# Optimization experiments

Hardware: AMD Instinct MI355X
Metric: run time of the kernel (lower is better)

## Reference

```python
import jax, jax.numpy as jnp
import numpy as np

C, W = 144, 9225          # channel_count, batch_width
KW, F = 10, 64            # kernel_width, fc_segment_length
H1 = 128                  # second layer out
CAT = 2 * C * F           # 18432 = C*F (fc) + (W-KW+1) (conv)


def setup_inputs() -> dict:
    key = jax.random.key(0)
    ks = jax.random.split(key, 9)
    s_fc = 1.0 / np.sqrt(W)
    s_cv = 1.0 / np.sqrt(C * KW)
    s_1 = 1.0 / np.sqrt(CAT)
    s_2 = 1.0 / np.sqrt(H1)
    return {
        "x":     jax.random.normal(ks[0], (C, W), jnp.float32),
        "Wfc":   jax.random.normal(ks[1], (C, F, W), jnp.float32) * s_fc,
        "bfc":   jax.random.normal(ks[2], (C, F), jnp.float32) * s_fc,
        "Kconv": jax.random.normal(ks[3], (C, KW), jnp.float32) * s_cv,
        "bconv": jax.random.normal(ks[4], (1,), jnp.float32) * s_cv,
        "W1":    jax.random.normal(ks[5], (H1, CAT), jnp.float32) * s_1,
        "b1":    jax.random.normal(ks[6], (H1,), jnp.float32) * s_1,
        "W2":    jax.random.normal(ks[7], (1, H1), jnp.float32) * s_2,
        "b2":    jax.random.normal(ks[8], (1,), jnp.float32) * s_2,
    }


def reference(x, Wfc, bfc, Kconv, bconv, W1, b1, W2, b2):
    # 144 per-channel Linear(W->F) fused into one batched GEMV (no ReLU on
    # these in the original forward, despite the docstring).
    fc_out = (jnp.einsum('cfw,cw->cf', Wfc, x) + bfc).reshape(-1)  # [C*F]
    # Conv2d(1,1,(C,KW)): kernel height == channel count -> 1D valid corr.
    conv = jax.lax.conv_general_dilated(
        x[None, None],            # [1,1,C,W]
        Kconv[None, None],        # [1,1,C,KW]
        window_strides=(1, 1), padding='VALID')[0, 0, 0] + bconv  # [W-KW+1]
    concatenated = jnp.concatenate([fc_out, conv])                # [CAT]
    second = jax.nn.relu(W1 @ concatenated + b1)                  # [H1]
    out = jax.nn.relu(W2 @ second + b2)                           # [1]
    return jax.nn.sigmoid(out)
```

## Files before the change

### kernel.cpp

```cpp
#include <hip/hip_runtime.h>
#include <math.h>

#define CC    144
#define WW    9225
#define KWW   10
#define FF    64
#define H1N   128
#define CONVN (WW - KWW + 1)
#define CFN   (CC * FF)
#define CATN  (CFN + CONVN)
#define FCB2  (CC * 8)
#define NV4   36
#define NTAIL 9

typedef float f32x4  __attribute__((ext_vector_type(4)));
typedef float f32x4u __attribute__((ext_vector_type(4), aligned(4)));

__global__ __launch_bounds__(256) void k_front_v13(
    const float* __restrict__ x,
    const float* __restrict__ Wfc,
    const float* __restrict__ bfc,
    const float* __restrict__ Kc,
    const float* __restrict__ bconv,
    float* __restrict__ concat)
{
    __shared__ float smem[CC * KWW];
    const int bid = blockIdx.x;
    const int tid = threadIdx.x;

    if (bid < FCB2) {
        const int c = bid >> 3;
        const int g = bid & 7;
        const int wave = tid >> 6;
        const int lane = tid & 63;
        const int f0   = g * 8 + wave * 2;
        const int r0   = (c << 6) + f0;
        const f32x4u* __restrict__ w0v =
            (const f32x4u*)(Wfc + (size_t)r0 * WW);
        const f32x4u* __restrict__ w1v =
            (const f32x4u*)(Wfc + (size_t)(r0 + 1) * WW);
        const f32x4u* __restrict__ xv =
            (const f32x4u*)(x + (size_t)c * WW);

        float a0 = 0.f, a1 = 0.f;
        #pragma unroll 4
        for (int i = 0; i < NV4; ++i) {
            const int q = i * 64 + lane;
            const f32x4 xq = xv[q];
            const f32x4 wq0 = __builtin_nontemporal_load(w0v + q);
            const f32x4 wq1 = __builtin_nontemporal_load(w1v + q);
            a0 += wq0.x * xq.x + wq0.y * xq.y + wq0.z * xq.z + wq0.w * xq.w;
            a1 += wq1.x * xq.x + wq1.y * xq.y + wq1.z * xq.z + wq1.w * xq.w;
        }
        if (lane < NTAIL) {
            const int e = NV4 * 256 + lane;
            const float* __restrict__ xr = x + (size_t)c * WW;
            const float* __restrict__ wb = Wfc + (size_t)r0 * WW;
            a0 = fmaf(wb[e],      xr[e], a0);
            a1 = fmaf(wb[WW + e], xr[e], a1);
        }

        #pragma unroll
        for (int off = 32; off > 0; off >>= 1) {
            a0 += __shfl_xor(a0, off, 64);
            a1 += __shfl_xor(a1, off, 64);
        }
        if (lane == 0) {
            concat[r0]     = a0 + bfc[r0];
            concat[r0 + 1] = a1 + bfc[r0 + 1];
        }
    } else {
        for (int i = tid; i < CC * KWW; i += 256) smem[i] = Kc[i];
        __syncthreads();

        const int p = (bid - FCB2) * 256 + tid;
        float acc = bconv[0];
        for (int c = 0; c < CC; ++c) {
            const float* __restrict__ xr = x + (size_t)c * WW + p;
            const float* __restrict__ kr = smem + c * KWW;
            #pragma unroll
            for (int k = 0; k < KWW; ++k)
                acc = fmaf(xr[k], kr[k], acc);
        }
        concat[CFN + p] = acc;
    }
}

__global__ __launch_bounds__(256) void k_layer1_v2(
    const float* __restrict__ W1,
    const float* __restrict__ concat,
    float* __restrict__ partial)
{
    __shared__ float sm[4];
    const int j = blockIdx.x, tid = threadIdx.x;
    const int h = j >> 1, half = j & 1;
    const f32x4* __restrict__ wr =
        (const f32x4*)(W1 + (size_t)h * CATN + half * (CATN / 2));
    const f32x4* __restrict__ cv =
        (const f32x4*)(concat + half * (CATN / 2));

    float acc = 0.f;
    for (int i = tid; i < CATN / 8; i += 256) {
        const f32x4 a = wr[i];
        const f32x4 q = cv[i];
        acc += a.x * q.x + a.y * q.y + a.z * q.z + a.w * q.w;
    }
    #pragma unroll
    for (int off = 32; off > 0; off >>= 1)
        acc += __shfl_xor(acc, off, 64);
    if ((tid & 63) == 0) sm[tid >> 6] = acc;
    __syncthreads();
    if (tid == 0)
        partial[j] = sm[0] + sm[1] + sm[2] + sm[3];
}

__global__ __launch_bounds__(128) void k_final_v2(
    const float* __restrict__ partial,
    const float* __restrict__ b1,
    const float* __restrict__ W2,
    const float* __restrict__ b2,
    float* __restrict__ out)
{
    __shared__ float sm[2];
    const int tid = threadIdx.x;
    float v = fmaxf(partial[2 * tid] + partial[2 * tid + 1] + b1[tid], 0.f)
              * W2[tid];
    #pragma unroll
    for (int off = 32; off > 0; off >>= 1)
        v += __shfl_xor(v, off, 64);
    if ((tid & 63) == 0) sm[tid >> 6] = v;
    __syncthreads();
    if (tid == 0) {
        float z = sm[0] + sm[1] + b2[0];
        z = fmaxf(z, 0.f);
        out[0] = 1.f / (1.f + expf(-z));
    }
}

extern "C" void kernel_launch(void* const* d_in, const int* in_sizes, int n_in,
                              void* d_out, int out_size, void* d_ws, size_t ws_size,
                              hipStream_t stream) {
    const float* x     = (const float*)d_in[0];
    const float* Wfc   = (const float*)d_in[1];
    const float* bfc   = (const float*)d_in[2];
    const float* Kc    = (const float*)d_in[3];
    const float* bconv = (const float*)d_in[4];
    const float* W1    = (const float*)d_in[5];
    const float* b1    = (const float*)d_in[6];
    const float* W2    = (const float*)d_in[7];
    const float* b2    = (const float*)d_in[8];
    float* out = (float*)d_out;

    float* concat  = (float*)d_ws;
    float* partial = concat + CATN;

    k_front_v13<<<FCB2 + (CONVN / 256), 256, 0, stream>>>(
        x, Wfc, bfc, Kc, bconv, concat);
    k_layer1_v2<<<256, 256, 0, stream>>>(W1, concat, partial);
    k_final_v2 <<<1, 128, 0, stream>>>(partial, b1, W2, b2, out);
}
```

Baseline: 77.67 us.

## Fuse layer-1 GEMV and final head into front kernel via atomics

Folds the layer-1 matvec into the front kernel. Each FC wave multiplies its two outputs by the matching W1 columns, and each conv block multiplies its 256 conv outputs by the matching W1 slice. Partial sums go into a global pre-activation buffer with atomicAdd. A completion counter lets the last block finish, and that block applies bias, ReLU, W2 and sigmoid. This removes the concat round trip and the separate layer-1 and final launches, but W1 is now read with column-strided, uncoalesced accesses, and 128 addresses see heavy atomic contention.

Result: slower. 288.8 us (+271.8%).

```diff
diff --git a/kernel.cpp b/kernel.cpp
--- a/kernel.cpp
+++ b/kernel.cpp
@@ -10,43 +10,57 @@
 #define CFN   (CC * FF)
 #define CATN  (CFN + CONVN)
 #define FCB2  (CC * 8)
+#define CONVB (CONVN / 256)
+#define TOTB  (FCB2 + CONVB)
 #define NV4   36
 #define NTAIL 9
 
 typedef float f32x4  __attribute__((ext_vector_type(4)));
 typedef float f32x4u __attribute__((ext_vector_type(4), aligned(4)));
 
-__global__ __launch_bounds__(256) void k_front_v13(
+__global__ __launch_bounds__(256) void k_zero(float* pre1, unsigned* counter) {
+    const int tid = threadIdx.x;
+    if (tid < H1N) pre1[tid] = 0.f;
+    if (tid == 0) *counter = 0u;
+}
+
+__global__ __launch_bounds__(256) void k_fused(
     const float* __restrict__ x,
     const float* __restrict__ Wfc,
     const float* __restrict__ bfc,
     const float* __restrict__ Kc,
     const float* __restrict__ bconv,
-    float* __restrict__ concat)
+    const float* __restrict__ W1,
+    const float* __restrict__ b1,
+    const float* __restrict__ W2,
+    const float* __restrict__ b2,
+    float* __restrict__ pre1,
+    unsigned* __restrict__ counter,
+    float* __restrict__ out)
 {
-    __shared__ float smem[CC * KWW];
-    const int bid = blockIdx.x;
-    const int tid = threadIdx.x;
+    __shared__ float kc[CC * KWW];
+    __shared__ float p1[4][H1N];
+    __shared__ float convout[256];
+    __shared__ float smr[4];
+    __shared__ unsigned lastFlag;
+
+    const int bid  = blockIdx.x;
+    const int tid  = threadIdx.x;
+    const int wave = tid >> 6, lane = tid & 63;
 
     if (bid < FCB2) {
-        const int c = bid >> 3;
-        const int g = bid & 7;
-        const int wave = tid >> 6;
-        const int lane = tid & 63;
-        const int f0   = g * 8 + wave * 2;
-        const int r0   = (c << 6) + f0;
-        const f32x4u* __restrict__ w0v =
-            (const f32x4u*)(Wfc + (size_t)r0 * WW);
-        const f32x4u* __restrict__ w1v =
-            (const f32x4u*)(Wfc + (size_t)(r0 + 1) * WW);
-        const f32x4u* __restrict__ xv =
-            (const f32x4u*)(x + (size_t)c * WW);
+        const int c  = bid >> 3, g = bid & 7;
+        const int f0 = g * 8 + wave * 2;
+        const int r0 = (c << 6) + f0;
+        const f32x4u* __restrict__ w0v = (const f32x4u*)(Wfc + (size_t)r0 * WW);
+        const f32x4u* __restrict__ w1v = (const f32x4u*)(Wfc + (size_t)(r0 + 1) * WW);
+        const f32x4u* __restrict__ xv  = (const f32x4u*)(x + (size_t)c * WW);
 
         float a0 = 0.f, a1 = 0.f;
         #pragma unroll 4
         for (int i = 0; i < NV4; ++i) {
             const int q = i * 64 + lane;
-            const f32x4 xq = xv[q];
+            const f32x4 xq  = xv[q];
             const f32x4 wq0 = __builtin_nontemporal_load(w0v + q);
             const f32x4 wq1 = __builtin_nontemporal_load(w1v + q);
             a0 += wq0.x * xq.x + wq0.y * xq.y + wq0.z * xq.z + wq0.w * xq.w;
@@ -59,81 +73,79 @@
             a0 = fmaf(wb[e],      xr[e], a0);
             a1 = fmaf(wb[WW + e], xr[e], a1);
         }
-
         #pragma unroll
-        for (int off = 32; off > 0; off >>= 1) {
+        for (int off = 32; off; off >>= 1) {
             a0 += __shfl_xor(a0, off, 64);
             a1 += __shfl_xor(a1, off, 64);
         }
-        if (lane == 0) {
-            concat[r0]     = a0 + bfc[r0];
-            concat[r0 + 1] = a1 + bfc[r0 + 1];
+        a0 += bfc[r0];
+        a1 += bfc[r0 + 1];
+
+        {
+            const float* __restrict__ w1c = W1 + r0;
+            const size_t o0 = (size_t)lane * CATN;
+            const size_t o1 = (size_t)(lane + 64) * CATN;
+            p1[wave][lane]      = a0 * w1c[o0] + a1 * w1c[o0 + 1];
+            p1[wave][lane + 64] = a0 * w1c[o1] + a1 * w1c[o1 + 1];
         }
+        __syncthreads();
+        if (tid < H1N)
+            atomicAdd(&pre1[tid],
+                      p1[0][tid] + p1[1][tid] + p1[2][tid] + p1[3][tid]);
     } else {
-        for (int i = tid; i < CC * KWW; i += 256) smem[i] = Kc[i];
+        for (int i = tid; i < CC * KWW; i += 256) kc[i] = Kc[i];
         __syncthreads();
-
-        const int p = (bid - FCB2) * 256 + tid;
+        const int pbase = (bid - FCB2) * 256;
+        const int p = pbase + tid;
         float acc = bconv[0];
-        for (int c = 0; c < CC; ++c) {
-            const float* __restrict__ xr = x + (size_t)c * WW + p;
-            const float* __restrict__ kr = smem + c * KWW;
+        for (int c2 = 0; c2 < CC; ++c2) {
+            const float* __restrict__ xr = x + (size_t)c2 * WW + p;
+            const float* __restrict__ kr = kc + c2 * KWW;
             #pragma unroll
             for (int k = 0; k < KWW; ++k)
                 acc = fmaf(xr[k], kr[k], acc);
         }
-        concat[CFN + p] = acc;
+        convout[tid] = acc;
+        __syncthreads();
+        {
+            const int h = tid & 127, half = tid >> 7;
+            const float* __restrict__ wrow =
+                W1 + (size_t)h * CATN + CFN + pbase + half * 128;
+            const float* __restrict__ cvo = convout + half * 128;
+            float s = 0.f;
+            #pragma unroll 4
+            for (int j = 0; j < 128; ++j)
+                s = fmaf(cvo[j], wrow[j], s);
+            p1[half][h] = s;
+        }
+        __syncthreads();
+        if (tid < H1N)
+            atomicAdd(&pre1[tid], p1[0][tid] + p1[1][tid]);
     }
-}
 
-__global__ __launch_bounds__(256) void k_layer1_v2(
-    const float* __restrict__ W1,
-    const float* __restrict__ concat,
-    float* __restrict__ partial)
-{
-    __shared__ float sm[4];
-    const int j = blockIdx.x, tid = threadIdx.x;
-    const int h = j >> 1, half = j & 1;
-    const f32x4* __restrict__ wr =
-        (const f32x4*)(W1 + (size_t)h * CATN + half * (CATN / 2));
-    const f32x4* __restrict__ cv =
-        (const f32x4*)(concat + half * (CATN / 2));
-
-    float acc = 0.f;
-    for (int i = tid; i < CATN / 8; i += 256) {
-        const f32x4 a = wr[i];
-        const f32x4 q = cv[i];
-        acc += a.x * q.x + a.y * q.y + a.z * q.z + a.w * q.w;
-    }
-    #pragma unroll
-    for (int off = 32; off > 0; off >>= 1)
-        acc += __shfl_xor(acc, off, 64);
-    if ((tid & 63) == 0) sm[tid >> 6] = acc;
-    __syncthreads();
-    if (tid == 0)
-        partial[j] = sm[0] + sm[1] + sm[2] + sm[3];
-}
-
-__global__ __launch_bounds__(128) void k_final_v2(
-    const float* __restrict__ partial,
-    const float* __restrict__ b1,
-    const float* __restrict__ W2,
-    const float* __restrict__ b2,
-    float* __restrict__ out)
-{
-    __shared__ float sm[2];
-    const int tid = threadIdx.x;
-    float v = fmaxf(partial[2 * tid] + partial[2 * tid + 1] + b1[tid], 0.f)
-              * W2[tid];
-    #pragma unroll
-    for (int off = 32; off > 0; off >>= 1)
-        v += __shfl_xor(v, off, 64);
-    if ((tid & 63) == 0) sm[tid >> 6] = v;
+    __threadfence();
     __syncthreads();
     if (tid == 0) {
-        float z = sm[0] + sm[1] + b2[0];
-        z = fmaxf(z, 0.f);
-        out[0] = 1.f / (1.f + expf(-z));
+        const unsigned old = atomicAdd(counter, 1u);
+        lastFlag = (old == TOTB - 1) ? 1u : 0u;
+    }
+    __syncthreads();
+    if (lastFlag) {
+        float v = 0.f;
+        if (tid < H1N) {
+            const float pv = atomicAdd(&pre1[tid], 0.f);
+            v = fmaxf(pv + b1[tid], 0.f) * W2[tid];
+        }
+        #pragma unroll
+        for (int off = 32; off; off >>= 1)
+            v += __shfl_xor(v, off, 64);
+        if (lane == 0) smr[wave] = v;
+        __syncthreads();
+        if (tid == 0) {
+            float z = smr[0] + smr[1] + smr[2] + smr[3];
+            z = fmaxf(z + b2[0], 0.f);
+            out[0] = 1.f / (1.f + expf(-z));
+        }
     }
 }
 
@@ -151,11 +163,10 @@
     const float* b2    = (const float*)d_in[8];
     float* out = (float*)d_out;
 
-    float* concat  = (float*)d_ws;
-    float* partial = concat + CATN;
+    float*    pre1    = (float*)d_ws;
+    unsigned* counter = (unsigned*)(pre1 + H1N);
 
-    k_front_v13<<<FCB2 + (CONVN / 256), 256, 0, stream>>>(
-        x, Wfc, bfc, Kc, bconv, concat);
-    k_layer1_v2<<<256, 256, 0, stream>>>(W1, concat, partial);
-    k_final_v2 <<<1, 128, 0, stream>>>(partial, b1, W2, b2, out);
+    k_zero <<<1, 256, 0, stream>>>(pre1, counter);
+    k_fused<<<TOTB, 256, 0, stream>>>(x, Wfc, bfc, Kc, bconv,
+                                      W1, b1, W2, b2, pre1, counter, out);
 }
```
